# Kernel optimization log

Measured on AMD Instinct MI355X. Metric: run time of the kernel, lower is better.

Reference implementation:

```python
import jax, jax.numpy as jnp
import numpy as np

N = 50000      # nodes
E = 600000     # edges (before self-loops)
F_IN = 128     # num_node_features
HID = 64       # hidden_channels
HEADS = 4      # num_heads
ACT = 32       # action_dim
SENT = 768     # sentence embedding dim (fc1 input)


def setup_inputs() -> dict:
    key = jax.random.key(0)
    ks = jax.random.split(key, 32)
    rn = lambda k, s, sc=0.05: jax.random.normal(k, s, jnp.float32) * sc
    return {
        "x": jax.random.normal(ks[0], (N, F_IN), jnp.float32),
        "edge_index": jax.random.randint(ks[1], (2, E), 0, N, dtype=jnp.int32),
        "sentence_emb": jax.random.normal(ks[2], (1, SENT), jnp.float32),
        "active_node_idx": 123,
        "step": 3,
        # conv1: GATConv(F_IN -> HID, heads=HEADS, concat=True)
        "W1": rn(ks[3], (F_IN, HEADS * HID)),
        "att_src1": rn(ks[4], (HEADS, HID)),
        "att_dst1": rn(ks[5], (HEADS, HID)),
        "b1": jnp.zeros((HEADS * HID,), jnp.float32),
        # conv2: GATConv(HEADS*HID -> HID, heads=1, concat=False)
        "W2": rn(ks[6], (HEADS * HID, HID)),
        "att_src2": rn(ks[7], (1, HID)),
        "att_dst2": rn(ks[8], (1, HID)),
        "b2": jnp.zeros((HID,), jnp.float32),
        "fc0_w": rn(ks[9], (1, HID)), "fc0_b": jnp.zeros((HID,), jnp.float32),
        "fc1_w": rn(ks[10], (SENT, HID)), "fc1_b": jnp.zeros((HID,), jnp.float32),
        "fc2_w": rn(ks[11], (HID, HID)), "fc2_b": jnp.zeros((HID,), jnp.float32),
        "fc3_w": rn(ks[12], (2 * HID, HID)), "fc3_b": jnp.zeros((HID,), jnp.float32),
        "val_w": rn(ks[13], (HID, 1)), "val_b": jnp.zeros((1,), jnp.float32),
        "adv_w": rn(ks[14], (HID, ACT)), "adv_b": jnp.zeros((ACT,), jnp.float32),
        "ln_h_g": jnp.ones((HID,), jnp.float32), "ln_h_b": jnp.zeros((HID,), jnp.float32),
        "ln_f_g": jnp.ones((2 * HID,), jnp.float32), "ln_f_b": jnp.zeros((2 * HID,), jnp.float32),
        "ln_a_g": jnp.ones((HEADS * HID,), jnp.float32), "ln_a_b": jnp.zeros((HEADS * HID,), jnp.float32),
    }


def layernorm(x, g, b, eps=1e-5):
    mu = jnp.mean(x, axis=-1, keepdims=True)
    var = jnp.mean((x - mu) ** 2, axis=-1, keepdims=True)
    return (x - mu) / jnp.sqrt(var + eps) * g + b


def gat_layer(h_in, src, dst, W, a_src, a_dst, bias, concat):
    """PyG GATConv (eval mode): gather -> edge score -> segment softmax -> scatter-add."""
    n = h_in.shape[0]
    heads, ch = a_src.shape
    h = (h_in @ W).reshape(n, heads, ch)                      # [N,H,C]
    es = jnp.einsum('nhc,hc->nh', h, a_src)                   # alpha_src per node
    ed = jnp.einsum('nhc,hc->nh', h, a_dst)                   # alpha_dst per node
    e = jax.nn.leaky_relu(es[src] + ed[dst], 0.2)             # [Etot,H]
    m = jax.ops.segment_max(e, dst, num_segments=n)           # stable softmax per dst
    ex = jnp.exp(e - m[dst])
    denom = jax.ops.segment_sum(ex, dst, num_segments=n) + 1e-16
    alpha = ex / denom[dst]                                   # [Etot,H]
    out = jax.ops.segment_sum(h[src] * alpha[:, :, None], dst, num_segments=n)
    out = out.reshape(n, heads * ch) if concat else out.mean(axis=1)
    return out + bias, alpha


def reference(x, edge_index, sentence_emb, active_node_idx, step,
              W1, att_src1, att_dst1, b1, W2, att_src2, att_dst2, b2,
              fc0_w, fc0_b, fc1_w, fc1_b, fc2_w, fc2_b, fc3_w, fc3_b,
              val_w, val_b, adv_w, adv_b,
              ln_h_g, ln_h_b, ln_f_g, ln_f_b, ln_a_g, ln_a_b):
    n = x.shape[0]
    loops = jnp.arange(n, dtype=edge_index.dtype)             # PyG add_self_loops=True
    src = jnp.concatenate([edge_index[0], loops])
    dst = jnp.concatenate([edge_index[1], loops])

    # step embedding: fc0((step+1)*0.01) -> relu -> LN
    steps = jnp.full((1, 1), (step + 1) * 0.01, jnp.float32)
    steps = layernorm(jax.nn.relu(steps @ fc0_w + fc0_b), ln_h_g, ln_h_b)

    # sentence embedding path (F.normalize result is discarded in the original)
    sent = layernorm(jax.nn.relu(sentence_emb @ fc1_w + fc1_b), ln_h_g, ln_h_b)
    sent = sent + steps
    sent = layernorm(jax.nn.relu(sent @ fc2_w + fc2_b), ln_h_g, ln_h_b)

    # two GAT layers
    h1, _ = gat_layer(x, src, dst, W1, att_src1, att_dst1, b1, concat=True)
    h1 = layernorm(jax.nn.elu(h1), ln_a_g, ln_a_b)
    h2, alpha = gat_layer(h1, src, dst, W2, att_src2, att_dst2, b2, concat=False)
    h2 = layernorm(h2, ln_h_g, ln_h_b)

    # dueling head on active node
    anf = jnp.concatenate([h2[active_node_idx][None, :], sent], axis=1)   # [1, 2*HID]
    anf = layernorm(anf, ln_f_g, ln_f_b)
    anf = layernorm(jax.nn.relu(anf @ fc3_w + fc3_b), ln_h_g, ln_h_b)
    val = anf @ val_w + val_b
    adv = anf @ adv_w + adv_b
    logits = jnp.tanh(val + adv - adv.mean())
    return logits, h2, alpha
```

## Files before the change

### kernel.cpp

```cpp
#include <hip/hip_runtime.h>
#include <cstdint>
#include <cstddef>

#define DEV __device__ __forceinline__

static constexpr int NN  = 50000;
static constexpr int EE  = 600000;
static constexpr int ET  = 650000;
static constexpr int CAP = 96;

static constexpr int GEMM_BLOCKS = (NN + 63) / 64;
static constexpr int BF_BLOCKS   = (ET + 255) / 256;

typedef __attribute__((ext_vector_type(8))) short bf16x8;
typedef __attribute__((ext_vector_type(4))) float f32x4;
typedef __attribute__((ext_vector_type(4))) int   i32x4;

DEV float wsum(float v){
  #pragma unroll
  for (int o = 32; o > 0; o >>= 1) v += __shfl_xor(v, o, 64);
  return v;
}
DEV float lrelu(float x){ return x > 0.f ? x : 0.2f * x; }
DEV float eluf(float x){ return x > 0.f ? x : expm1f(x); }
DEV float ln64(float v, const float* g, const float* b, int lane){
  float mu  = wsum(v) * (1.f/64.f);
  float d   = v - mu;
  float var = wsum(d*d) * (1.f/64.f);
  return d * rsqrtf(var + 1e-5f) * g[lane] + b[lane];
}
DEV unsigned int bf16u(float f){
  unsigned int u = __float_as_uint(f);
  return (u + 0x7fffu + ((u >> 16) & 1u)) >> 16;
}
DEV float bfl(unsigned int lo16){ return __uint_as_float(lo16 << 16); }

__global__ __launch_bounds__(256) void pack_both(const float* __restrict__ W1,
                                                 const float* __restrict__ W2,
                                                 short* __restrict__ Wp1,
                                                 short* __restrict__ Wp2){
  int tid = blockIdx.x * 256 + threadIdx.x;
  if (tid < 4096){
    int lane = tid & 63, ks = (tid >> 6) & 3, mb = tid >> 8;
    int col  = mb * 16 + (lane & 15);
    int krow = ks * 32 + (lane >> 4) * 8;
    #pragma unroll
    for (int j = 0; j < 8; j++)
      Wp1[(size_t)tid * 8 + j] = (short)bf16u(W1[(size_t)(krow + j) * 256 + col]);
  } else if (tid < 4096 + 2048){
    int t2 = tid - 4096;
    int lane = t2 & 63, ks = (t2 >> 6) & 7, mb = t2 >> 9;
    int col  = mb * 16 + (lane & 15);
    int krow = ks * 32 + (lane >> 4) * 8;
    #pragma unroll
    for (int j = 0; j < 8; j++)
      Wp2[(size_t)t2 * 8 + j] = (short)bf16u(W2[(size_t)(krow + j) * 64 + col]);
  }
}

template<int KSTEPS, int MBLKS, int NH, bool INF32>
DEV void gemm_body(int blk,
                   const short* __restrict__ Wp,
                   const float* __restrict__ Xf,
                   const unsigned short* __restrict__ Xh,
                   unsigned short* __restrict__ Cb,
                   const float* __restrict__ asrc,
                   const float* __restrict__ adst,
                   float* __restrict__ es,
                   float* __restrict__ ed, int M){
  constexpr int K = KSTEPS * 32, N = MBLKS * 16;
  int lane  = threadIdx.x & 63;
  int wv    = threadIdx.x >> 6;
  int quad  = lane >> 4;
  int node  = blk * 64 + wv * 16 + (lane & 15);
  bool nv   = node < M;
  int nodec = nv ? node : M - 1;

  f32x4 acc[MBLKS];
  #pragma unroll
  for (int m = 0; m < MBLKS; m++) acc[m] = (f32x4){0.f, 0.f, 0.f, 0.f};

  #pragma unroll
  for (int ks = 0; ks < KSTEPS; ks++){
    int k0 = ks * 32 + quad * 8;
    bf16x8 bfrag;
    if (INF32){
      float4 u = *(const float4*)(Xf + (size_t)nodec * K + k0);
      float4 v = *(const float4*)(Xf + (size_t)nodec * K + k0 + 4);
      i32x4 bi;
      bi.x = (int)(bf16u(u.x) | (bf16u(u.y) << 16));
      bi.y = (int)(bf16u(u.z) | (bf16u(u.w) << 16));
      bi.z = (int)(bf16u(v.x) | (bf16u(v.y) << 16));
      bi.w = (int)(bf16u(v.z) | (bf16u(v.w) << 16));
      bfrag = __builtin_bit_cast(bf16x8, bi);
    } else {
      bfrag = *(const bf16x8*)(Xh + (size_t)nodec * K + k0);
    }
    #pragma unroll
    for (int mb = 0; mb < MBLKS; mb++){
      bf16x8 afrag = *(const bf16x8*)(Wp + ((size_t)(mb * KSTEPS + ks) * 64 + lane) * 8);
      acc[mb] = __builtin_amdgcn_mfma_f32_16x16x32_bf16(afrag, bfrag, acc[mb], 0, 0, 0);
    }
  }

  if (nv){
    unsigned short* crow = Cb + (size_t)node * N;
    #pragma unroll
    for (int mb = 0; mb < MBLKS; mb++){
      uint2 p;
      p.x = bf16u(acc[mb][0]) | (bf16u(acc[mb][1]) << 16);
      p.y = bf16u(acc[mb][2]) | (bf16u(acc[mb][3]) << 16);
      *(uint2*)(crow + mb * 16 + quad * 4) = p;
    }
  }

  float ps[NH], pd[NH];
  #pragma unroll
  for (int h = 0; h < NH; h++){ ps[h] = 0.f; pd[h] = 0.f; }
  #pragma unroll
  for (int mb = 0; mb < MBLKS; mb++){
    int h = (NH == 1) ? 0 : (mb >> 2);
    #pragma unroll
    for (int r = 0; r < 4; r++){
      int c = mb * 16 + quad * 4 + r;
      ps[h] = fmaf(acc[mb][r], asrc[c], ps[h]);
      pd[h] = fmaf(acc[mb][r], adst[c], pd[h]);
    }
  }
  #pragma unroll
  for (int h = 0; h < NH; h++){
    ps[h] += __shfl_xor(ps[h], 16, 64); ps[h] += __shfl_xor(ps[h], 32, 64);
    pd[h] += __shfl_xor(pd[h], 16, 64); pd[h] += __shfl_xor(pd[h], 32, 64);
  }
  if (quad == 0 && nv){
    if (NH == 4){
      *(float4*)(es + (size_t)node * 4) = make_float4(ps[0], ps[1], ps[2], ps[3]);
      *(float4*)(ed + (size_t)node * 4) = make_float4(pd[0], pd[1], pd[2], pd[3]);
    } else {
      es[node] = ps[0];
      ed[node] = pd[0];
    }
  }
}

__global__ __launch_bounds__(256) void fused_front(const short* __restrict__ Wp1,
                                                   const float* __restrict__ x,
                                                   unsigned short* __restrict__ H1b,
                                                   const float* __restrict__ as1,
                                                   const float* __restrict__ ad1,
                                                   float* __restrict__ es1,
                                                   float* __restrict__ ed1,
                                                   const int* __restrict__ ei,
                                                   int* __restrict__ cnt,
                                                   int* __restrict__ bucket){
  int b = blockIdx.x;
  if (b < GEMM_BLOCKS){
    gemm_body<4, 16, 4, true>(b, Wp1, x, nullptr, H1b, as1, ad1, es1, ed1, NN);
  } else {
    int e = (b - GEMM_BLOCKS) * 256 + threadIdx.x;
    if (e < ET){
      int src, dst;
      if (e < EE){ src = ei[e]; dst = ei[EE + e]; } else { src = dst = e - EE; }
      int pos = atomicAdd(&cnt[dst], 1);
      if (pos < CAP) bucket[(size_t)dst * CAP + pos] = src;
    }
  }
}

template<int KSTEPS, int MBLKS, int NH, bool INF32>
__global__ __launch_bounds__(256) void mfma_gemm_att(const short* __restrict__ Wp,
                                                     const float* __restrict__ Xf,
                                                     const unsigned short* __restrict__ Xh,
                                                     unsigned short* __restrict__ Cb,
                                                     const float* __restrict__ asrc,
                                                     const float* __restrict__ adst,
                                                     float* __restrict__ es,
                                                     float* __restrict__ ed, int M){
  gemm_body<KSTEPS, MBLKS, NH, INF32>(blockIdx.x, Wp, Xf, Xh, Cb, asrc, adst, es, ed, M);
}

DEV void acc4u(uint2 g, float q, float& ax, float& ay, float& az, float& aw){
  ax = fmaf(__uint_as_float(g.x << 16),         q, ax);
  ay = fmaf(__uint_as_float(g.x & 0xffff0000u), q, ay);
  az = fmaf(__uint_as_float(g.y << 16),         q, az);
  aw = fmaf(__uint_as_float(g.y & 0xffff0000u), q, aw);
}

__global__ __launch_bounds__(256) void agg1_kernel(const int* __restrict__ cnt,
                                                   const int* __restrict__ bucket,
                                                   const unsigned short* __restrict__ H1b,
                                                   const float* __restrict__ es,
                                                   const float* __restrict__ ed,
                                                   const float* __restrict__ b1,
                                                   const float* __restrict__ lng,
                                                   const float* __restrict__ lnb,
                                                   unsigned short* __restrict__ h1b, int n){
  __shared__ float wsh4[4][64][4];
  __shared__ int   ssh[4][64];
  int wv   = threadIdx.x >> 6;
  int wid  = (blockIdx.x * blockDim.x + threadIdx.x) >> 6;
  int lane = threadIdx.x & 63;
  if (wid >= n) return;
  int deg = min(cnt[wid], CAP);
  const int* base = bucket + (size_t)wid * CAP;
  const float4 edv = *(const float4*)(ed + (size_t)wid * 4);

  float v0, v1, v2, v3;

  if (deg <= 64){
    bool vld = lane < deg;
    int srcl = vld ? base[lane] : 0;
    float4 e4 = vld ? *(const float4*)(es + (size_t)srcl * 4)
                    : make_float4(0.f, 0.f, 0.f, 0.f);
    float w0 = vld ? __expf(lrelu(e4.x + edv.x)) : 0.f;
    float w1 = vld ? __expf(lrelu(e4.y + edv.y)) : 0.f;
    float w2 = vld ? __expf(lrelu(e4.z + edv.z)) : 0.f;
    float w3 = vld ? __expf(lrelu(e4.w + edv.w)) : 0.f;
    ssh[wv][lane] = srcl;
    *(float4*)&wsh4[wv][lane][0] = make_float4(w0, w1, w2, w3);
    __builtin_amdgcn_wave_barrier();

    int h = lane >> 4;
    int lane4 = lane * 4;
    float ax = 0.f, ay = 0.f, az = 0.f, aw = 0.f;
    int t = 0;
    for (; t + 4 <= deg; t += 4){
      int a0 = ssh[wv][t],     a1 = ssh[wv][t + 1];
      int a2 = ssh[wv][t + 2], a3 = ssh[wv][t + 3];
      float q0 = wsh4[wv][t][h],     q1 = wsh4[wv][t + 1][h];
      float q2 = wsh4[wv][t + 2][h], q3 = wsh4[wv][t + 3][h];
      uint2 g0 = *(const uint2*)(H1b + (size_t)a0 * 256 + lane4);
      uint2 g1 = *(const uint2*)(H1b + (size_t)a1 * 256 + lane4);
      uint2 g2 = *(const uint2*)(H1b + (size_t)a2 * 256 + lane4);
      uint2 g3 = *(const uint2*)(H1b + (size_t)a3 * 256 + lane4);
      acc4u(g0, q0, ax, ay, az, aw);
      acc4u(g1, q1, ax, ay, az, aw);
      acc4u(g2, q2, ax, ay, az, aw);
      acc4u(g3, q3, ax, ay, az, aw);
    }
    for (; t < deg; t++){
      int a0 = ssh[wv][t];
      float q0 = wsh4[wv][t][h];
      uint2 g0 = *(const uint2*)(H1b + (size_t)a0 * 256 + lane4);
      acc4u(g0, q0, ax, ay, az, aw);
    }
    float den0 = wsum(w0) + 1e-16f;
    float den1 = wsum(w1) + 1e-16f;
    float den2 = wsum(w2) + 1e-16f;
    float den3 = wsum(w3) + 1e-16f;
    float denh = (h < 2) ? (h == 0 ? den0 : den1) : (h == 2 ? den2 : den3);
    float rden = __builtin_amdgcn_rcpf(denh);
    float4 bb = *(const float4*)(b1 + lane4);
    v0 = eluf(fmaf(ax, rden, bb.x)); v1 = eluf(fmaf(ay, rden, bb.y));
    v2 = eluf(fmaf(az, rden, bb.z)); v3 = eluf(fmaf(aw, rden, bb.w));
    float s1 = wsum(v0 + v1 + v2 + v3);
    float s2 = wsum(fmaf(v0, v0, fmaf(v1, v1, fmaf(v2, v2, v3 * v3))));
    float mu   = s1 * (1.f/256.f);
    float rstd = rsqrtf(fmaf(-mu, mu, s2 * (1.f/256.f)) + 1e-5f);
    float4 g4v = *(const float4*)(lng + lane4);
    float4 bo  = *(const float4*)(lnb + lane4);
    uint2 p;
    p.x = bf16u((v0-mu)*rstd*g4v.x + bo.x) | (bf16u((v1-mu)*rstd*g4v.y + bo.y) << 16);
    p.y = bf16u((v2-mu)*rstd*g4v.z + bo.z) | (bf16u((v3-mu)*rstd*g4v.w + bo.w) << 16);
    *(uint2*)(h1b + (size_t)wid * 256 + lane4) = p;
    return;
  }

  float acc0 = 0.f, acc1 = 0.f, acc2 = 0.f, acc3 = 0.f;
  float den0 = 0.f, den1 = 0.f, den2 = 0.f, den3 = 0.f;
  for (int j = 0; j < deg; j++){
    int src = base[j];
    float4 e4 = *(const float4*)(es + (size_t)src * 4);
    float x0 = __expf(lrelu(e4.x + edv.x));
    float x1 = __expf(lrelu(e4.y + edv.y));
    float x2 = __expf(lrelu(e4.z + edv.z));
    float x3 = __expf(lrelu(e4.w + edv.w));
    den0 += x0; den1 += x1; den2 += x2; den3 += x3;
    const unsigned short* hp = H1b + (size_t)src * 256;
    acc0 = fmaf(bfl(hp[lane]),       x0, acc0);
    acc1 = fmaf(bfl(hp[64 + lane]),  x1, acc1);
    acc2 = fmaf(bfl(hp[128 + lane]), x2, acc2);
    acc3 = fmaf(bfl(hp[192 + lane]), x3, acc3);
  }
  v0 = eluf(acc0 / (den0 + 1e-16f) + b1[lane]);
  v1 = eluf(acc1 / (den1 + 1e-16f) + b1[64 + lane]);
  v2 = eluf(acc2 / (den2 + 1e-16f) + b1[128 + lane]);
  v3 = eluf(acc3 / (den3 + 1e-16f) + b1[192 + lane]);
  float s1 = wsum(v0 + v1 + v2 + v3);
  float s2 = wsum(fmaf(v0, v0, fmaf(v1, v1, fmaf(v2, v2, v3 * v3))));
  float mu   = s1 * (1.f/256.f);
  float rstd = rsqrtf(fmaf(-mu, mu, s2 * (1.f/256.f)) + 1e-5f);
  unsigned short* o = h1b + (size_t)wid * 256;
  o[lane]       = (unsigned short)bf16u((v0-mu)*rstd*lng[lane]       + lnb[lane]);
  o[64 + lane]  = (unsigned short)bf16u((v1-mu)*rstd*lng[64 + lane]  + lnb[64 + lane]);
  o[128 + lane] = (unsigned short)bf16u((v2-mu)*rstd*lng[128 + lane] + lnb[128 + lane]);
  o[192 + lane] = (unsigned short)bf16u((v3-mu)*rstd*lng[192 + lane] + lnb[192 + lane]);
}

DEV float agg2_slow(const int* base, int deg, float edv,
                    const unsigned short* H2b, const float* es,
                    int lane, float& rden_out){
  float den = 0.f;
  for (int j = lane; j < deg; j += 64)
    den += __expf(lrelu(es[base[j]] + edv));
  den = wsum(den) + 1e-16f;
  float rden = __builtin_amdgcn_rcpf(den);
  float acc = 0.f;
  for (int j = 0; j < deg; j++){
    int src = base[j];
    float a = __expf(lrelu(es[src] + edv));
    acc = fmaf(bfl(H2b[(size_t)src * 64 + lane]), a, acc);
  }
  rden_out = rden;
  return acc * rden;
}

__global__ __launch_bounds__(256) void agg2_head(const int* __restrict__ cnt,
                                                 const int* __restrict__ bucket,
                                                 const unsigned short* __restrict__ H2b,
                                                 const float* __restrict__ es,
                                                 const float* __restrict__ ed,
                                                 const float* __restrict__ b2,
                                                 const float* __restrict__ lng,
                                                 const float* __restrict__ lnb,
                                                 const float* __restrict__ semb,
                                                 const int* __restrict__ active,
                                                 const int* __restrict__ stepp,
                                                 const float* __restrict__ fc0w, const float* __restrict__ fc0b,
                                                 const float* __restrict__ fc1w, const float* __restrict__ fc1b,
                                                 const float* __restrict__ fc2w, const float* __restrict__ fc2b,
                                                 const float* __restrict__ fc3w, const float* __restrict__ fc3b,
                                                 const float* __restrict__ valw, const float* __restrict__ valb,
                                                 const float* __restrict__ advw, const float* __restrict__ advb,
                                                 const float* __restrict__ lnhg, const float* __restrict__ lnhb,
                                                 const float* __restrict__ lnfg, const float* __restrict__ lnfb,
                                                 float* __restrict__ h2out,
                                                 float2* __restrict__ mden,
                                                 float* __restrict__ logits, int n){
  __shared__ float shh[192];
  __shared__ int   ssh[4][64];
  __shared__ float wsh[4][64];
  int wv   = threadIdx.x >> 6;
  int node = (blockIdx.x * blockDim.x + threadIdx.x) >> 6;
  int lane = threadIdx.x & 63;
  if (node >= n) return;

  int p  = lane >> 5;
  int c0 = (lane & 31) * 2;

  int deg = min(cnt[node], CAP);
  const int* base = bucket + (size_t)node * CAP;
  float edv = ed[node];

  float2 a = make_float2(0.f, 0.f);

  if (deg <= 64){
    bool vld = lane < deg;
    int s0 = vld ? base[lane] : 0;
    float w0 = vld ? __expf(lrelu(es[s0] + edv)) : 0.f;
    ssh[wv][lane] = s0;
    wsh[wv][lane] = w0;
    __builtin_amdgcn_wave_barrier();

    int dpad = (deg + 7) & ~7;
    for (int t = 0; t < dpad; t += 8){
      int   i0 = ssh[wv][t     + p], i1 = ssh[wv][t + 2 + p];
      int   i2 = ssh[wv][t + 4 + p], i3 = ssh[wv][t + 6 + p];
      float q0 = wsh[wv][t     + p], q1 = wsh[wv][t + 2 + p];
      float q2 = wsh[wv][t + 4 + p], q3 = wsh[wv][t + 6 + p];
      unsigned int g0 = *(const unsigned int*)(H2b + (size_t)i0 * 64 + c0);
      unsigned int g1 = *(const unsigned int*)(H2b + (size_t)i1 * 64 + c0);
      unsigned int g2 = *(const unsigned int*)(H2b + (size_t)i2 * 64 + c0);
      unsigned int g3 = *(const unsigned int*)(H2b + (size_t)i3 * 64 + c0);
      a.x = fmaf(__uint_as_float(g0 << 16),         q0, a.x);
      a.y = fmaf(__uint_as_float(g0 & 0xffff0000u), q0, a.y);
      a.x = fmaf(__uint_as_float(g1 << 16),         q1, a.x);
      a.y = fmaf(__uint_as_float(g1 & 0xffff0000u), q1, a.y);
      a.x = fmaf(__uint_as_float(g2 << 16),         q2, a.x);
      a.y = fmaf(__uint_as_float(g2 & 0xffff0000u), q2, a.y);
      a.x = fmaf(__uint_as_float(g3 << 16),         q3, a.x);
      a.y = fmaf(__uint_as_float(g3 & 0xffff0000u), q3, a.y);
    }
    float den = wsum(w0) + 1e-16f;
    float rden = __builtin_amdgcn_rcpf(den);
    if (lane == 0) mden[node] = make_float2(0.f, rden);
    a.x += __shfl_xor(a.x, 32, 64);
    a.y += __shfl_xor(a.y, 32, 64);
    a.x *= rden; a.y *= rden;
  } else {
    float rden;
    float accc = agg2_slow(base, deg, edv, H2b, es, lane, rden);
    if (lane == 0) mden[node] = make_float2(0.f, rden);
    a.x = __shfl(accc, c0, 64);
    a.y = __shfl(accc, c0 + 1, 64);
  }

  float2 bb = *(const float2*)(b2 + c0);
  float vx = a.x + bb.x, vy = a.y + bb.y;
  float s1 = wsum(vx + vy);
  float s2 = wsum(fmaf(vx, vx, vy * vy));
  float mu = s1 * (1.f/128.f);
  float rs = rsqrtf(fmaf(-mu, mu, s2 * (1.f/128.f)) + 1e-5f);
  float dx = vx - mu, dy = vy - mu;
  float2 gg = *(const float2*)(lng + c0);
  float2 bo = *(const float2*)(lnb + c0);
  float hx = dx * rs * gg.x + bo.x;
  float hy = dy * rs * gg.y + bo.y;
  if (p == 0) *(float2*)(h2out + (size_t)node * 64 + c0) = make_float2(hx, hy);

  if (node == active[0]){
    if (p == 0) *(float2*)&shh[128 + c0] = make_float2(hx, hy);
    __builtin_amdgcn_wave_barrier();
    int t = lane;
    float h2v = shh[128 + t];
    __builtin_amdgcn_wave_barrier();

    float sval = (float)(stepp[0] + 1) * 0.01f;
    float stepsv = ln64(fmaxf(fmaf(sval, fc0w[t], fc0b[t]), 0.f), lnhg, lnhb, t);

    float acc1h = fc1b[t];
    #pragma unroll 8
    for (int k = 0; k < 768; k++) acc1h = fmaf(semb[k], fc1w[k * 64 + t], acc1h);
    float sentv = ln64(fmaxf(acc1h, 0.f), lnhg, lnhb, t) + stepsv;
    shh[t] = sentv;
    __builtin_amdgcn_wave_barrier();
    float acc2h = fc2b[t];
    #pragma unroll 8
    for (int k = 0; k < 64; k++) acc2h = fmaf(shh[k], fc2w[k * 64 + t], acc2h);
    __builtin_amdgcn_wave_barrier();
    float sent2 = ln64(fmaxf(acc2h, 0.f), lnhg, lnhb, t);

    float c0h = h2v, c1h = sent2;
    float mu2 = wsum(c0h + c1h) * (1.f/128.f);
    float q2  = (c0h-mu2)*(c0h-mu2) + (c1h-mu2)*(c1h-mu2);
    float rs2 = rsqrtf(wsum(q2) * (1.f/128.f) + 1e-5f);
    shh[t]      = (c0h-mu2)*rs2*lnfg[t]      + lnfb[t];
    shh[64 + t] = (c1h-mu2)*rs2*lnfg[64 + t] + lnfb[64 + t];
    __builtin_amdgcn_wave_barrier();

    float acc3h = fc3b[t];
    #pragma unroll 8
    for (int k = 0; k < 128; k++) acc3h = fmaf(shh[k], fc3w[k * 64 + t], acc3h);
    float a2v = ln64(fmaxf(acc3h, 0.f), lnhg, lnhb, t);
    shh[128 + t] = a2v;
    __builtin_amdgcn_wave_barrier();

    float val = wsum(a2v * valw[t]) + valb[0];
    float advv = 0.f;
    if (t < 32){
      advv = advb[t];
      #pragma unroll 8
      for (int k = 0; k < 64; k++) advv = fmaf(shh[128 + k], advw[k * 32 + t], advv);
    }
    float am = wsum(t < 32 ? advv : 0.f) * (1.f/32.f);
    if (t < 32) logits[t] = tanhf(val + advv - am);
  }
}

__global__ __launch_bounds__(256) void edge_alpha(const int* __restrict__ ei,
                                                  const float* __restrict__ es,
                                                  const float* __restrict__ ed,
                                                  const float2* __restrict__ mden,
                                                  float* __restrict__ alpha_out){
  int e = blockIdx.x * blockDim.x + threadIdx.x;
  if (e >= ET) return;
  int src, dst;
  if (e < EE){ src = ei[e]; dst = ei[EE + e]; } else { src = dst = e - EE; }
  float2 md = mden[dst];
  float sc = lrelu(es[src] + ed[dst]);
  alpha_out[e] = __expf(sc) * md.y;
}

extern "C" void kernel_launch(void* const* d_in, const int* in_sizes, int n_in,
                              void* d_out, int out_size, void* d_ws, size_t ws_size,
                              hipStream_t stream) {
  const float* x     = (const float*)d_in[0];
  const int*   ei    = (const int*)  d_in[1];
  const float* semb  = (const float*)d_in[2];
  const int*   act   = (const int*)  d_in[3];
  const int*   step  = (const int*)  d_in[4];
  const float* W1    = (const float*)d_in[5];
  const float* as1   = (const float*)d_in[6];
  const float* ad1   = (const float*)d_in[7];
  const float* b1    = (const float*)d_in[8];
  const float* W2    = (const float*)d_in[9];
  const float* as2   = (const float*)d_in[10];
  const float* ad2   = (const float*)d_in[11];
  const float* b2    = (const float*)d_in[12];
  const float* fc0w  = (const float*)d_in[13];
  const float* fc0b  = (const float*)d_in[14];
  const float* fc1w  = (const float*)d_in[15];
  const float* fc1b  = (const float*)d_in[16];
  const float* fc2w  = (const float*)d_in[17];
  const float* fc2b  = (const float*)d_in[18];
  const float* fc3w  = (const float*)d_in[19];
  const float* fc3b  = (const float*)d_in[20];
  const float* valw  = (const float*)d_in[21];
  const float* valb  = (const float*)d_in[22];
  const float* advw  = (const float*)d_in[23];
  const float* advb  = (const float*)d_in[24];
  const float* lnhg  = (const float*)d_in[25];
  const float* lnhb  = (const float*)d_in[26];
  const float* lnfg  = (const float*)d_in[27];
  const float* lnfb  = (const float*)d_in[28];
  const float* lnag  = (const float*)d_in[29];
  const float* lnab  = (const float*)d_in[30];

  char* ws = (char*)d_ws;
  size_t o = 0;
  auto alloc = [&](size_t bytes) -> void* {
    o = (o + 255) & ~(size_t)255;
    void* p = ws + o;
    o += bytes;
    return p;
  };
  int*   cnt     = (int*)  alloc((size_t)NN * 4);
  int*   bucket  = (int*)  alloc((size_t)NN * CAP * 4);
  short* Wp1     = (short*)alloc((size_t)4096 * 8 * 2);
  short* Wp2     = (short*)alloc((size_t)2048 * 8 * 2);
  unsigned short* H1b = (unsigned short*)alloc((size_t)NN * 256 * 2);
  unsigned short* h1b = (unsigned short*)alloc((size_t)NN * 256 * 2);
  float* es1     = (float*)alloc((size_t)NN * 16);
  float* ed1     = (float*)alloc((size_t)NN * 16);
  float2* mden   = (float2*)alloc((size_t)NN * 8);
  unsigned short* H2b = H1b;
  float* es2 = es1;
  float* ed2 = ed1;

  float* logits    = (float*)d_out;
  float* h2out     = (float*)d_out + 32;
  float* alpha_out = (float*)d_out + 32 + (size_t)NN * 64;

  hipMemsetAsync(cnt, 0, (size_t)NN * 4, stream);
  pack_both<<<24, 256, 0, stream>>>(W1, W2, Wp1, Wp2);

  fused_front<<<GEMM_BLOCKS + BF_BLOCKS, 256, 0, stream>>>(
      Wp1, x, H1b, as1, ad1, es1, ed1, ei, cnt, bucket);

  agg1_kernel<<<NN / 4, 256, 0, stream>>>(cnt, bucket, H1b, es1, ed1, b1, lnag, lnab, h1b, NN);

  mfma_gemm_att<8, 4, 1, false><<<GEMM_BLOCKS, 256, 0, stream>>>(
      Wp2, nullptr, h1b, H2b, as2, ad2, es2, ed2, NN);
  agg2_head<<<(NN + 3) / 4, 256, 0, stream>>>(cnt, bucket, H2b, es2, ed2, b2,
                                              lnhg, lnhb,
                                              semb, act, step,
                                              fc0w, fc0b, fc1w, fc1b, fc2w, fc2b, fc3w, fc3b,
                                              valw, valb, advw, advb,
                                              lnhg, lnhb, lnfg, lnfb,
                                              h2out, mden, logits, NN);
  edge_alpha<<<(ET + 255) / 256, 256, 0, stream>>>(ei, es2, ed2, mden, alpha_out);
}
```

Before: 335.2 us.

## Stage GEMM input tile through LDS with coalesced loads; reorder fused front blocks

The GEMM body now loads each block's 64-row input tile cooperatively into padded shared memory with fully coalesced 16-byte loads (converting fp32 to bf16 on the way), then reads MFMA B-fragments from LDS. Before, each lane read strided 16-byte pieces of its row straight from global memory. The fused front kernel also puts the edge-bucketing blocks first so the atomic-heavy work is dispatched ahead of the GEMM blocks. The LDS tile adds a barrier and uses shared memory, which may lower occupancy; the gain depends on whether the original global access pattern was actually inefficient.

```diff
diff --git a/kernel.cpp b/kernel.cpp
--- a/kernel.cpp
+++ b/kernel.cpp
@@ -14,7 +14,6 @@
 
 typedef __attribute__((ext_vector_type(8))) short bf16x8;
 typedef __attribute__((ext_vector_type(4))) float f32x4;
-typedef __attribute__((ext_vector_type(4))) int   i32x4;
 
 DEV float wsum(float v){
   #pragma unroll
@@ -68,34 +67,49 @@
                    const float* __restrict__ adst,
                    float* __restrict__ es,
                    float* __restrict__ ed, int M){
-  constexpr int K = KSTEPS * 32, N = MBLKS * 16;
-  int lane  = threadIdx.x & 63;
-  int wv    = threadIdx.x >> 6;
+  constexpr int K  = KSTEPS * 32, N = MBLKS * 16;
+  constexpr int XS = K + 8;
+  constexpr int CH = K / 8;
+  constexpr int ITERS = 64 * CH / 256;
+  __shared__ unsigned short xs[64][XS];
+
+  int tid   = threadIdx.x;
+  int lane  = tid & 63;
+  int wv    = tid >> 6;
   int quad  = lane >> 4;
   int node  = blk * 64 + wv * 16 + (lane & 15);
   bool nv   = node < M;
-  int nodec = nv ? node : M - 1;
+
+  #pragma unroll
+  for (int it = 0; it < ITERS; it++){
+    int c  = it * 256 + tid;
+    int g  = c / CH;
+    int ko = (c % CH) * 8;
+    int grow = min(blk * 64 + g, M - 1);
+    if (INF32){
+      float4 u = *(const float4*)(Xf + (size_t)grow * K + ko);
+      float4 v = *(const float4*)(Xf + (size_t)grow * K + ko + 4);
+      uint4 pk;
+      pk.x = bf16u(u.x) | (bf16u(u.y) << 16);
+      pk.y = bf16u(u.z) | (bf16u(u.w) << 16);
+      pk.z = bf16u(v.x) | (bf16u(v.y) << 16);
+      pk.w = bf16u(v.z) | (bf16u(v.w) << 16);
+      *(uint4*)&xs[g][ko] = pk;
+    } else {
+      *(uint4*)&xs[g][ko] = *(const uint4*)(Xh + (size_t)grow * K + ko);
+    }
+  }
+  __syncthreads();
 
   f32x4 acc[MBLKS];
   #pragma unroll
   for (int m = 0; m < MBLKS; m++) acc[m] = (f32x4){0.f, 0.f, 0.f, 0.f};
 
+  int lrow = wv * 16 + (lane & 15);
   #pragma unroll
   for (int ks = 0; ks < KSTEPS; ks++){
     int k0 = ks * 32 + quad * 8;
-    bf16x8 bfrag;
-    if (INF32){
-      float4 u = *(const float4*)(Xf + (size_t)nodec * K + k0);
-      float4 v = *(const float4*)(Xf + (size_t)nodec * K + k0 + 4);
-      i32x4 bi;
-      bi.x = (int)(bf16u(u.x) | (bf16u(u.y) << 16));
-      bi.y = (int)(bf16u(u.z) | (bf16u(u.w) << 16));
-      bi.z = (int)(bf16u(v.x) | (bf16u(v.y) << 16));
-      bi.w = (int)(bf16u(v.z) | (bf16u(v.w) << 16));
-      bfrag = __builtin_bit_cast(bf16x8, bi);
-    } else {
-      bfrag = *(const bf16x8*)(Xh + (size_t)nodec * K + k0);
-    }
+    bf16x8 bfrag = *(const bf16x8*)&xs[lrow][k0];
     #pragma unroll
     for (int mb = 0; mb < MBLKS; mb++){
       bf16x8 afrag = *(const bf16x8*)(Wp + ((size_t)(mb * KSTEPS + ks) * 64 + lane) * 8);
@@ -154,16 +168,16 @@
                                                    int* __restrict__ cnt,
                                                    int* __restrict__ bucket){
   int b = blockIdx.x;
-  if (b < GEMM_BLOCKS){
-    gemm_body<4, 16, 4, true>(b, Wp1, x, nullptr, H1b, as1, ad1, es1, ed1, NN);
-  } else {
-    int e = (b - GEMM_BLOCKS) * 256 + threadIdx.x;
+  if (b < BF_BLOCKS){
+    int e = b * 256 + threadIdx.x;
     if (e < ET){
       int src, dst;
       if (e < EE){ src = ei[e]; dst = ei[EE + e]; } else { src = dst = e - EE; }
       int pos = atomicAdd(&cnt[dst], 1);
       if (pos < CAP) bucket[(size_t)dst * CAP + pos] = src;
     }
+  } else {
+    gemm_body<4, 16, 4, true>(b - BF_BLOCKS, Wp1, x, nullptr, H1b, as1, ad1, es1, ed1, NN);
   }
 }
 
@@ -534,7 +548,7 @@
   hipMemsetAsync(cnt, 0, (size_t)NN * 4, stream);
   pack_both<<<24, 256, 0, stream>>>(W1, W2, Wp1, Wp2);
 
-  fused_front<<<GEMM_BLOCKS + BF_BLOCKS, 256, 0, stream>>>(
+  fused_front<<<BF_BLOCKS + GEMM_BLOCKS, 256, 0, stream>>>(
       Wp1, x, H1b, as1, ad1, es1, ed1, ei, cnt, bucket);
 
   agg1_kernel<<<NN / 4, 256, 0, stream>>>(cnt, bucket, H1b, es1, ed1, b1, lnag, lnab, h1b, NN);
```

Measured after the change: 340.5 us. No clear change (+1.6%).
